# Optimization experiments

Hardware: AMD Instinct MI355X
Metric: run time of the kernel (lower is better)

The kernel has to match this reference:

```python
import jax, jax.numpy as jnp
import numpy as np

LMAX = 2
NEG_SLOPE = 0.2
N, K = 8192, 32
C_IN, C_ATTN = 128, 128
HEADS, HDIM = 8, 32
RAD_CH = [128, 64, 64, 2 * C_ATTN * (LMAX + 1)]  # edge_channel_list + [768]

# e3nn real spherical harmonics, normalize=True, normalization='integral'
_C0 = 0.28209479177387814           # sqrt(1/(4*pi))
_C1 = 0.4886025119029199            # sqrt(3/(4*pi))
_C2 = 0.6307831305050401            # sqrt(5/(4*pi))
_S3 = 1.7320508075688772            # sqrt(3)

def _sh(l, u):
    x, y, z = u[..., 0], u[..., 1], u[..., 2]
    if l == 0:
        return jnp.full(u.shape[:-1] + (1,), _C0, dtype=u.dtype)
    if l == 1:
        return _C1 * jnp.stack([x, y, z], axis=-1)
    return _C2 * jnp.stack([
        _S3 * x * z,
        _S3 * x * y,
        y * y - 0.5 * (x * x + z * z),
        _S3 * y * z,
        0.5 * _S3 * (z * z - x * x),
    ], axis=-1)

def _layernorm(x, g, b, eps=1e-5):
    m = jnp.mean(x, axis=-1, keepdims=True)
    v = jnp.var(x, axis=-1, keepdims=True)
    return (x - m) * jax.lax.rsqrt(v + eps) * g + b

def _smooth_leaky_relu(x):
    # (1+a)/2 * x + (1-a)/2 * x * (2*sigmoid(x) - 1)
    return 0.5 * (1 + NEG_SLOPE) * x + 0.5 * (1 - NEG_SLOPE) * x * (2.0 * jax.nn.sigmoid(x) - 1.0)


def setup_inputs() -> dict:
    key = jax.random.key(0)
    ks = jax.random.split(key, 32)
    inp = {}
    inp['x_edge'] = jax.random.normal(ks[0], (N, K, RAD_CH[0]), jnp.float32)
    inp['node_irreps_input'] = jax.random.normal(ks[1], (N, (LMAX + 1) ** 2, C_IN), jnp.float32)
    inp['edge_vec'] = jax.random.normal(ks[2], (N, K, 3), jnp.float32)
    inp['f_sparse_idx_node'] = jax.random.randint(ks[3], (N, K), 0, N)
    # SO3_Linear: per-l weight [lmax+1, out, in], bias only for l=0
    inp['dot_w'] = jax.random.normal(ks[4], (LMAX + 1, C_ATTN, C_IN), jnp.float32) / np.sqrt(C_IN)
    inp['dot_b'] = jnp.zeros((C_ATTN,), jnp.float32)
    # RadialFunction: Linear-LN-SiLU, Linear-LN-SiLU, Linear
    for i in range(3):
        inp[f'rad_w{i}'] = jax.random.normal(ks[5 + i], (RAD_CH[i + 1], RAD_CH[i]), jnp.float32) / np.sqrt(RAD_CH[i])
        inp[f'rad_b{i}'] = jnp.zeros((RAD_CH[i + 1],), jnp.float32)
    for i in range(2):
        inp[f'rad_g{i}'] = jnp.ones((RAD_CH[i + 1],), jnp.float32)
        inp[f'rad_bb{i}'] = jnp.zeros((RAD_CH[i + 1],), jnp.float32)
    # fc_m0: 768 -> heads*head
    inp['fc_w'] = jax.random.normal(ks[10], (HEADS * HDIM, RAD_CH[-1]), jnp.float32) / np.sqrt(RAD_CH[-1])
    inp['fc_b'] = jnp.zeros((HEADS * HDIM,), jnp.float32)
    # alpha_norm (LayerNorm over attn_scalar_head)
    inp['ln_g'] = jnp.ones((HDIM,), jnp.float32)
    inp['ln_b'] = jnp.zeros((HDIM,), jnp.float32)
    # alpha_dot ~ U(-1/sqrt(head), 1/sqrt(head))
    std = 1.0 / np.sqrt(HDIM)
    inp['alpha_dot'] = jax.random.uniform(ks[11], (HEADS, HDIM), jnp.float32, -std, std)
    return inp


def reference(x_edge, node_irreps_input, edge_vec, f_sparse_idx_node,
              dot_w, dot_b, rad_w0, rad_b0, rad_w1, rad_b1, rad_w2, rad_b2,
              rad_g0, rad_bb0, rad_g1, rad_bb1, fc_w, fc_b, ln_g, ln_b, alpha_dot):
    n = node_irreps_input.shape[0]
    # normalize edge vectors (e3nn normalize=True)
    u = edge_vec / jnp.clip(jnp.linalg.norm(edge_vec, axis=-1, keepdims=True), 1e-12)
    feats = []
    for l in range(LMAX + 1):
        node_l = node_irreps_input[:, l * l:(l + 1) * (l + 1)]          # [N, 2l+1, C_in]
        node_l = jnp.einsum('nmc,dc->nmd', node_l, dot_w[l])            # [N, 2l+1, C_attn]
        if l == 0:
            node_l = node_l + dot_b
        sh = _sh(l, u)                                                   # [N, K, 2l+1]
        feats.append(jnp.einsum('nkm,nmd->nkd', sh, node_l))            # self term
        gathered = jnp.take(node_l, f_sparse_idx_node, axis=0)          # [N, K, 2l+1, C_attn]
        feats.append(jnp.einsum('nkm,nkmd->nkd', sh, gathered))         # neighbor term
    x0 = jnp.concatenate(feats, axis=-1)                                 # [N, K, 768]
    # radial MLP on edge scalars
    h = jax.nn.silu(_layernorm(x_edge @ rad_w0.T + rad_b0, rad_g0, rad_bb0))
    h = jax.nn.silu(_layernorm(h @ rad_w1.T + rad_b1, rad_g1, rad_bb1))
    edge_m0 = h @ rad_w2.T + rad_b2                                      # [N, K, 768]
    x0a = (x0 * edge_m0) @ fc_w.T + fc_b                                 # [N, K, H*Dh]
    x0a = x0a.reshape(n, -1, HEADS, HDIM)
    x0a = _smooth_leaky_relu(_layernorm(x0a, ln_g, ln_b))
    alpha = jnp.einsum('nkhd,hd->nkh', x0a, alpha_dot)                   # [N, K, H]
    return alpha
```

## Files before the change

### kernel.cpp

```cpp
#include <hip/hip_runtime.h>
#include <hip/hip_bf16.h>
#include <stdint.h>

typedef __hip_bfloat16 bf16_t;
typedef __attribute__((ext_vector_type(8))) short bfrag8;
typedef __attribute__((ext_vector_type(4))) float facc4;

__device__ __forceinline__ float bfu(unsigned short s) {
  union { unsigned int i; float f; } u; u.i = ((unsigned int)s) << 16; return u.f;
}
__device__ __forceinline__ float2 bfup(unsigned int v) {
  union { unsigned int i; float f; } a, b;
  a.i = v << 16;
  b.i = v & 0xffff0000u;
  float2 r; r.x = a.f; r.y = b.f; return r;
}
__device__ __forceinline__ unsigned short f2b(float f) {
  __hip_bfloat16 h = __float2bfloat16(f);
  return *(unsigned short*)&h;
}
__device__ __forceinline__ void gload_lds16(const void* g, void* l) {
  __builtin_amdgcn_global_load_lds(
      (const __attribute__((address_space(1))) unsigned int*)g,
      (__attribute__((address_space(3))) unsigned int*)l, 16, 0, 0);
}

template<bool BF>
__device__ __forceinline__ float ld1(const void* p, size_t i) {
  if (BF) return bfu(((const unsigned short*)p)[i]);
  return ((const float*)p)[i];
}
template<bool BF>
__device__ __forceinline__ void ld8(const void* p, size_t i, float* o) {
  if (BF) {
    uint4 v = *(const uint4*)((const unsigned short*)p + i);
    float2 a = bfup(v.x), b = bfup(v.y), c = bfup(v.z), d = bfup(v.w);
    o[0]=a.x; o[1]=a.y; o[2]=b.x; o[3]=b.y; o[4]=c.x; o[5]=c.y; o[6]=d.x; o[7]=d.y;
  } else {
    float4 v0 = *(const float4*)((const float*)p + i);
    float4 v1 = *(const float4*)((const float*)p + i + 4);
    o[0]=v0.x; o[1]=v0.y; o[2]=v0.z; o[3]=v0.w; o[4]=v1.x; o[5]=v1.y; o[6]=v1.z; o[7]=v1.w;
  }
}
template<bool BF>
__device__ __forceinline__ void st1(void* p, size_t i, float v) {
  if (BF) ((unsigned short*)p)[i] = f2b(v);
  else    ((float*)p)[i] = v;
}
__device__ __forceinline__ bool tag_is_bf16(const void* ones) {
  return *(const unsigned int*)ones == 0x3F803F80u;
}

template<bool BF>
__global__ __launch_bounds__(256) void k_prep(
    const void* __restrict__ fcw, const void* __restrict__ w2,
    const void* __restrict__ lng,
    unsigned short* __restrict__ dstf, unsigned short* __restrict__ dstw2)
{
  if (tag_is_bf16(lng) != BF) return;
  int i = blockIdx.x * 256 + threadIdx.x;
  for (int e = i; e < 196608; e += 65536) dstf[e] = f2b(ld1<BF>(fcw, e));
  if (i < 49152) dstw2[i] = f2b(ld1<BF>(w2, i));
}

template<bool BF>
__global__ __launch_bounds__(128) void k_nodelin(
    const void* __restrict__ node, const void* __restrict__ dotw,
    const void* __restrict__ dotb, const void* __restrict__ lng,
    unsigned short* __restrict__ nlin)
{
  if (tag_is_bf16(lng) != BF) return;
  const int n = blockIdx.x, t = threadIdx.x;
  __shared__ alignas(16) float ns[1152];
  for (int i = t; i < 144; i += 128) ld8<BF>(node, (size_t)n * 1152 + i * 8, ns + i * 8);
  __syncthreads();
  unsigned short* outr = nlin + (size_t)n * 1152;
  #pragma unroll
  for (int l = 0; l < 3; ++l) {
    const int mb = l * l, mc = 2 * l + 1;
    float acc[5];
    #pragma unroll
    for (int mm = 0; mm < 5; ++mm) acc[mm] = 0.f;
    if (l == 0) acc[0] = ld1<BF>(dotb, t);
    #pragma unroll
    for (int c8 = 0; c8 < 16; ++c8) {
      float w[8]; ld8<BF>(dotw, (size_t)l * 16384 + (size_t)t * 128 + c8 * 8, w);
      #pragma unroll
      for (int mm = 0; mm < 5; ++mm) {
        if (mm < mc) {
          const float* sc = ns + (mb + mm) * 128 + c8 * 8;
          acc[mm] += sc[0]*w[0] + sc[1]*w[1] + sc[2]*w[2] + sc[3]*w[3]
                   + sc[4]*w[4] + sc[5]*w[5] + sc[6]*w[6] + sc[7]*w[7];
        }
      }
    }
    #pragma unroll
    for (int mm = 0; mm < 5; ++mm)
      if (mm < mc) outr[(mb + mm) * 128 + t] = f2b(acc[mm]);
  }
}

template<bool BF>
__global__ __launch_bounds__(256) void k_rad(
    const void* __restrict__ xe_g,
    const void* __restrict__ w0g, const void* __restrict__ b0g,
    const void* __restrict__ w1g, const void* __restrict__ b1g,
    const void* __restrict__ g0g, const void* __restrict__ bb0g,
    const void* __restrict__ g1g, const void* __restrict__ bb1g,
    const void* __restrict__ lng, unsigned short* __restrict__ h1g)
{
  if (tag_is_bf16(lng) != BF) return;
  const int t = threadIdx.x;
  const size_t ebase = (size_t)blockIdx.x * 64;
  __shared__ alignas(16) unsigned short xs [64 * 136];
  __shared__ alignas(16) unsigned short ws0[64 * 136];
  __shared__ alignas(16) unsigned short ws1[64 * 72];
  __shared__ alignas(16) unsigned short hs [64 * 72];

  for (int i8 = t; i8 < 1024; i8 += 256) {
    float v[8]; ld8<BF>(xe_g, (ebase + (i8 >> 4)) * 128 + (i8 & 15) * 8, v);
    unsigned short* d = &xs[(i8 >> 4) * 136 + (i8 & 15) * 8];
    #pragma unroll
    for (int j = 0; j < 8; ++j) d[j] = f2b(v[j]);
  }
  for (int i8 = t; i8 < 1024; i8 += 256) {
    float v[8]; ld8<BF>(w0g, (size_t)(i8 >> 4) * 128 + (i8 & 15) * 8, v);
    unsigned short* d = &ws0[(i8 >> 4) * 136 + (i8 & 15) * 8];
    #pragma unroll
    for (int j = 0; j < 8; ++j) d[j] = f2b(v[j]);
  }
  for (int i8 = t; i8 < 512; i8 += 256) {
    float v[8]; ld8<BF>(w1g, (size_t)(i8 >> 3) * 64 + (i8 & 7) * 8, v);
    unsigned short* d = &ws1[(i8 >> 3) * 72 + (i8 & 7) * 8];
    #pragma unroll
    for (int j = 0; j < 8; ++j) d[j] = f2b(v[j]);
  }
  __syncthreads();

  const int wv = t >> 6, lane = t & 63, la = lane & 15, qa = lane >> 4;
  facc4 acc[4];
  #pragma unroll
  for (int nt = 0; nt < 4; ++nt) acc[nt] = (facc4){0.f, 0.f, 0.f, 0.f};
  #pragma unroll
  for (int ks = 0; ks < 4; ++ks) {
    const int kk = ks * 32 + qa * 8;
    bfrag8 a = *(const bfrag8*)&xs[(wv * 16 + la) * 136 + kk];
    #pragma unroll
    for (int nt = 0; nt < 4; ++nt) {
      bfrag8 b = *(const bfrag8*)&ws0[(nt * 16 + la) * 136 + kk];
      acc[nt] = __builtin_amdgcn_mfma_f32_16x16x32_bf16(a, b, acc[nt], 0, 0, 0);
    }
  }
  {
    float bz[4], g[4], bb[4];
    #pragma unroll
    for (int nt = 0; nt < 4; ++nt) {
      const int ch = nt * 16 + la;
      bz[nt] = ld1<BF>(b0g, ch); g[nt] = ld1<BF>(g0g, ch); bb[nt] = ld1<BF>(bb0g, ch);
    }
    #pragma unroll
    for (int r = 0; r < 4; ++r) {
      float v[4], s = 0.f, s2 = 0.f;
      #pragma unroll
      for (int nt = 0; nt < 4; ++nt) { v[nt] = acc[nt][r] + bz[nt]; s += v[nt]; s2 += v[nt]*v[nt]; }
      #pragma unroll
      for (int msk = 1; msk < 16; msk <<= 1) { s += __shfl_xor(s, msk, 64); s2 += __shfl_xor(s2, msk, 64); }
      float mean = s * (1.f / 64.f);
      float var  = fmaxf(s2 * (1.f / 64.f) - mean * mean, 0.f);
      float rs   = rsqrtf(var + 1e-5f);
      const int er = wv * 16 + qa * 4 + r;
      #pragma unroll
      for (int nt = 0; nt < 4; ++nt) {
        float x = (v[nt] - mean) * rs * g[nt] + bb[nt];
        hs[er * 72 + nt * 16 + la] = f2b(x / (1.f + __expf(-x)));
      }
    }
  }
  __syncthreads();
  facc4 acc2[4];
  #pragma unroll
  for (int nt = 0; nt < 4; ++nt) acc2[nt] = (facc4){0.f, 0.f, 0.f, 0.f};
  #pragma unroll
  for (int ks = 0; ks < 2; ++ks) {
    const int kk = ks * 32 + qa * 8;
    bfrag8 a = *(const bfrag8*)&hs[(wv * 16 + la) * 72 + kk];
    #pragma unroll
    for (int nt = 0; nt < 4; ++nt) {
      bfrag8 b = *(const bfrag8*)&ws1[(nt * 16 + la) * 72 + kk];
      acc2[nt] = __builtin_amdgcn_mfma_f32_16x16x32_bf16(a, b, acc2[nt], 0, 0, 0);
    }
  }
  {
    float bz[4], g[4], bb[4];
    #pragma unroll
    for (int nt = 0; nt < 4; ++nt) {
      const int ch = nt * 16 + la;
      bz[nt] = ld1<BF>(b1g, ch); g[nt] = ld1<BF>(g1g, ch); bb[nt] = ld1<BF>(bb1g, ch);
    }
    #pragma unroll
    for (int r = 0; r < 4; ++r) {
      float v[4], s = 0.f, s2 = 0.f;
      #pragma unroll
      for (int nt = 0; nt < 4; ++nt) { v[nt] = acc2[nt][r] + bz[nt]; s += v[nt]; s2 += v[nt]*v[nt]; }
      #pragma unroll
      for (int msk = 1; msk < 16; msk <<= 1) { s += __shfl_xor(s, msk, 64); s2 += __shfl_xor(s2, msk, 64); }
      float mean = s * (1.f / 64.f);
      float var  = fmaxf(s2 * (1.f / 64.f) - mean * mean, 0.f);
      float rs   = rsqrtf(var + 1e-5f);
      const size_t er = ebase + wv * 16 + qa * 4 + r;
      #pragma unroll
      for (int nt = 0; nt < 4; ++nt) {
        float x = (v[nt] - mean) * rs * g[nt] + bb[nt];
        h1g[er * 64 + nt * 16 + la] = f2b(x / (1.f + __expf(-x)));
      }
    }
  }
}

template<bool BF>
__global__ __launch_bounds__(256, 4) void k_y(
    const void* __restrict__ evec, const int* __restrict__ idxg,
    const unsigned short* __restrict__ nlin, const unsigned short* __restrict__ h1g,
    const unsigned short* __restrict__ w2bf, const void* __restrict__ b2g,
    const void* __restrict__ lng,
    int node0, unsigned short* __restrict__ yg)
{
  if (tag_is_bf16(lng) != BF) return;
  const int nloc = blockIdx.x;
  const int n = node0 + nloc;
  const int t = threadIdx.x;
  __shared__ alignas(16) unsigned short h1_s[32 * 72];
  __shared__ alignas(16) float sh_s[32][9];
  __shared__ alignas(16) int idx_s[32];
  __shared__ alignas(16) float x0g[3][16 * 132];

  if (t < 32) {
    idx_s[t] = idxg[n * 32 + t];
    size_t eo = (size_t)(n * 32 + t) * 3;
    float x = ld1<BF>(evec, eo), y = ld1<BF>(evec, eo + 1), z = ld1<BF>(evec, eo + 2);
    float r = fmaxf(sqrtf(x * x + y * y + z * z), 1e-12f);
    float inv = 1.f / r; x *= inv; y *= inv; z *= inv;
    const float C1 = 0.4886025119029199f, C2 = 0.6307831305050401f, S3 = 1.7320508075688772f;
    sh_s[t][0] = 0.28209479177387814f;
    sh_s[t][1] = C1 * x; sh_s[t][2] = C1 * y; sh_s[t][3] = C1 * z;
    sh_s[t][4] = C2 * S3 * x * z;
    sh_s[t][5] = C2 * S3 * x * y;
    sh_s[t][6] = C2 * (y * y - 0.5f * (x * x + z * z));
    sh_s[t][7] = C2 * S3 * y * z;
    sh_s[t][8] = C2 * 0.5f * S3 * (z * z - x * x);
  }
  {
    int e = t >> 3, c = (t & 7) * 8;
    *(uint4*)&h1_s[e * 72 + c] = *(const uint4*)(h1g + ((size_t)n * 32 + e) * 64 + c);
  }
  __syncthreads();

  const int wv = t >> 6, lane = t & 63, la = lane & 15, qa = lane >> 4;
  const int dbase0 = wv * 192;
  unsigned short* yb = yg + (size_t)nloc * 32 * 768;

  #pragma unroll 1
  for (int half = 0; half < 2; ++half) {
    #pragma unroll 1
    for (int pass = 0; pass < 4; ++pass) {
      const int kl = pass * 4 + (t >> 6);
      const int ke = half * 16 + kl;
      const int dd0 = (t & 63) * 2;
      const unsigned short* rp = nlin + (size_t)idx_s[ke] * 1152 + dd0;
      const float* sh = sh_s[ke];
      unsigned int v; float2 f;
      v = *(const unsigned int*)(rp + 0 * 128); f = bfup(v);
      float s0x = sh[0] * f.x, s0y = sh[0] * f.y;
      v = *(const unsigned int*)(rp + 1 * 128); f = bfup(v);
      float s1x = sh[1] * f.x, s1y = sh[1] * f.y;
      v = *(const unsigned int*)(rp + 2 * 128); f = bfup(v);
      s1x += sh[2] * f.x; s1y += sh[2] * f.y;
      v = *(const unsigned int*)(rp + 3 * 128); f = bfup(v);
      s1x += sh[3] * f.x; s1y += sh[3] * f.y;
      v = *(const unsigned int*)(rp + 4 * 128); f = bfup(v);
      float s2x = sh[4] * f.x, s2y = sh[4] * f.y;
      v = *(const unsigned int*)(rp + 5 * 128); f = bfup(v);
      s2x += sh[5] * f.x; s2y += sh[5] * f.y;
      v = *(const unsigned int*)(rp + 6 * 128); f = bfup(v);
      s2x += sh[6] * f.x; s2y += sh[6] * f.y;
      v = *(const unsigned int*)(rp + 7 * 128); f = bfup(v);
      s2x += sh[7] * f.x; s2y += sh[7] * f.y;
      v = *(const unsigned int*)(rp + 8 * 128); f = bfup(v);
      s2x += sh[8] * f.x; s2y += sh[8] * f.y;
      float* p0 = &x0g[0][kl * 132 + dd0];
      float* p1 = &x0g[1][kl * 132 + dd0];
      float* p2 = &x0g[2][kl * 132 + dd0];
      p0[0] = s0x; p0[1] = s0y;
      p1[0] = s1x; p1[1] = s1y;
      p2[0] = s2x; p2[1] = s2y;
    }
    __syncthreads();

    const bfrag8 ah0 = *(const bfrag8*)&h1_s[(half * 16 + la) * 72 + qa * 8];
    const bfrag8 ah1 = *(const bfrag8*)&h1_s[(half * 16 + la) * 72 + 32 + qa * 8];
    #pragma unroll 1
    for (int nt = 0; nt < 12; ++nt) {
      const int d = dbase0 + nt * 16 + la;
      const int b = (dbase0 + nt * 16) >> 7;
      const int l = b >> 1;
      const bool gat = b & 1;
      const int mbase = l * l;
      const int mcnt = 2 * l + 1;
      const int dd = d & 127;

      facc4 acc = (facc4){0.f, 0.f, 0.f, 0.f};
      {
        bfrag8 bfr0 = *(const bfrag8*)(w2bf + (size_t)d * 64 + qa * 8);
        bfrag8 bfr1 = *(const bfrag8*)(w2bf + (size_t)d * 64 + 32 + qa * 8);
        acc = __builtin_amdgcn_mfma_f32_16x16x32_bf16(ah0, bfr0, acc, 0, 0, 0);
        acc = __builtin_amdgcn_mfma_f32_16x16x32_bf16(ah1, bfr1, acc, 0, 0, 0);
      }
      const float bias = ld1<BF>(b2g, d);

      if (!gat) {
        float pv[5];
        #pragma unroll
        for (int mm = 0; mm < 5; ++mm)
          pv[mm] = (mm < mcnt) ? bfu(nlin[(size_t)n * 1152 + (mbase + mm) * 128 + dd]) : 0.f;
        #pragma unroll
        for (int r = 0; r < 4; ++r) {
          const int kl = qa * 4 + r;
          const int ke = half * 16 + kl;
          float x0 = 0.f;
          #pragma unroll
          for (int mm = 0; mm < 5; ++mm)
            x0 += ((mm < mcnt) ? sh_s[ke][mbase + mm] : 0.f) * pv[mm];
          yb[(size_t)ke * 768 + d] = f2b(x0 * (acc[r] + bias));
        }
      } else {
        const float* xl = x0g[l];
        #pragma unroll
        for (int r = 0; r < 4; ++r) {
          const int kl = qa * 4 + r;
          const float x0 = xl[kl * 132 + dd];
          yb[(size_t)(half * 16 + kl) * 768 + d] = f2b(x0 * (acc[r] + bias));
        }
      }
    }
    __syncthreads();
  }
}

template<bool BF>
__global__ __launch_bounds__(256, 4) void k_fc2(
    const unsigned short* __restrict__ yg, const unsigned short* __restrict__ fcwbf,
    const void* __restrict__ fcb, const void* __restrict__ lng,
    const void* __restrict__ lnb, const void* __restrict__ adot,
    int node0, void* __restrict__ out)
{
  if (tag_is_bf16(lng) != BF) return;
  const int t = threadIdx.x;
  const int nb = blockIdx.y;
  __shared__ alignas(16) unsigned short a_s[128 * 64];
  __shared__ alignas(16) unsigned short b_s[128 * 64];

  const int wv = t >> 6, wm = wv >> 1, wn = wv & 1;
  const int lane = t & 63, la = lane & 15, qa = lane >> 4;
  const int lrow = lane >> 3, lg = lane & 7;

  facc4 acc[4][4];
  #pragma unroll
  for (int mt = 0; mt < 4; ++mt)
    #pragma unroll
    for (int nt = 0; nt < 4; ++nt) acc[mt][nt] = (facc4){0.f, 0.f, 0.f, 0.f};

  const unsigned short* abase = yg + (size_t)blockIdx.x * 128 * 768;
  const unsigned short* bbase = fcwbf + (size_t)nb * 128 * 768;

  #pragma unroll 1
  for (int kb = 0; kb < 12; ++kb) {
    #pragma unroll
    for (int j = 0; j < 4; ++j) {
      const int rbase = (wv * 4 + j) * 8;
      const int row = rbase + lrow;
      const int gs = (lg ^ (row & 7)) * 8;
      gload_lds16(abase + (size_t)row * 768 + kb * 64 + gs, &a_s[rbase * 64]);
    }
    #pragma unroll
    for (int j = 0; j < 4; ++j) {
      const int rbase = (wv * 4 + j) * 8;
      const int row = rbase + lrow;
      const int gs = (lg ^ (row & 7)) * 8;
      gload_lds16(bbase + (size_t)row * 768 + kb * 64 + gs, &b_s[rbase * 64]);
    }
    __syncthreads();
    #pragma unroll
    for (int ks = 0; ks < 2; ++ks) {
      const int g = ks * 4 + qa;
      bfrag8 af[4];
      #pragma unroll
      for (int mt = 0; mt < 4; ++mt) {
        const int ar = wm * 64 + mt * 16 + la;
        af[mt] = *(const bfrag8*)&a_s[ar * 64 + (g ^ (ar & 7)) * 8];
      }
      #pragma unroll
      for (int nt = 0; nt < 4; ++nt) {
        const int br = wn * 64 + nt * 16 + la;
        bfrag8 bf = *(const bfrag8*)&b_s[br * 64 + (g ^ (br & 7)) * 8];
        #pragma unroll
        for (int mt = 0; mt < 4; ++mt)
          acc[mt][nt] = __builtin_amdgcn_mfma_f32_16x16x32_bf16(af[mt], bf, acc[mt][nt], 0, 0, 0);
      }
    }
    __syncthreads();
  }

  const float gl0 = ld1<BF>(lng, la), gl1 = ld1<BF>(lng, la + 16);
  const float bl0 = ld1<BF>(lnb, la), bl1 = ld1<BF>(lnb, la + 16);
  const size_t e0 = (size_t)node0 * 32 + (size_t)blockIdx.x * 128 + wm * 64;
  #pragma unroll
  for (int hh = 0; hh < 2; ++hh) {
    const int hgl = nb * 4 + wn * 2 + hh;
    const float fb0 = ld1<BF>(fcb, hgl * 32 + la);
    const float fb1 = ld1<BF>(fcb, hgl * 32 + 16 + la);
    const float ad0 = ld1<BF>(adot, hgl * 32 + la);
    const float ad1 = ld1<BF>(adot, hgl * 32 + 16 + la);
    #pragma unroll
    for (int mt = 0; mt < 4; ++mt) {
      #pragma unroll
      for (int r = 0; r < 4; ++r) {
        float v0 = acc[mt][2 * hh][r] + fb0;
        float v1 = acc[mt][2 * hh + 1][r] + fb1;
        float s = v0 + v1, s2 = v0 * v0 + v1 * v1;
        #pragma unroll
        for (int msk = 1; msk < 16; msk <<= 1) {
          s  += __shfl_xor(s,  msk, 64);
          s2 += __shfl_xor(s2, msk, 64);
        }
        float mean = s * (1.f / 32.f);
        float var  = fmaxf(s2 * (1.f / 32.f) - mean * mean, 0.f);
        float rs   = rsqrtf(var + 1e-5f);
        float x0n = (v0 - mean) * rs * gl0 + bl0;
        float x1n = (v1 - mean) * rs * gl1 + bl1;
        float sg0 = 1.f / (1.f + __expf(-x0n));
        float sg1 = 1.f / (1.f + __expf(-x1n));
        float p = (0.6f * x0n + 0.4f * x0n * (2.f * sg0 - 1.f)) * ad0
                + (0.6f * x1n + 0.4f * x1n * (2.f * sg1 - 1.f)) * ad1;
        #pragma unroll
        for (int msk = 1; msk < 16; msk <<= 1) p += __shfl_xor(p, msk, 64);
        if (la == 0) {
          const size_t e = e0 + mt * 16 + qa * 4 + r;
          st1<BF>(out, e * 8 + hgl, p);
        }
      }
    }
  }
}

template<bool BF>
__global__ __launch_bounds__(256) void k_edge2(
    const void* __restrict__ evec, const int* __restrict__ idxg,
    const unsigned short* __restrict__ nlin, const unsigned short* __restrict__ fcwbf,
    const unsigned short* __restrict__ h1g,
    const void* __restrict__ w2g, const void* __restrict__ b2g,
    const void* __restrict__ fcb, const void* __restrict__ lng,
    const void* __restrict__ lnb, const void* __restrict__ adot,
    void* __restrict__ out)
{
  if (tag_is_bf16(lng) != BF) return;
  const int n = blockIdx.x, t = threadIdx.x;
  __shared__ alignas(16) unsigned short y_s[32 * 776];
  __shared__ alignas(16) unsigned short h1_s[32 * 72];
  __shared__ alignas(16) float sh_s[32][9];
  __shared__ alignas(16) int idx_s[32];

  if (t < 32) {
    idx_s[t] = idxg[n * 32 + t];
    size_t eo = (size_t)(n * 32 + t) * 3;
    float x = ld1<BF>(evec, eo), y = ld1<BF>(evec, eo + 1), z = ld1<BF>(evec, eo + 2);
    float r = fmaxf(sqrtf(x * x + y * y + z * z), 1e-12f);
    float inv = 1.f / r; x *= inv; y *= inv; z *= inv;
    const float C1 = 0.4886025119029199f, C2 = 0.6307831305050401f, S3 = 1.7320508075688772f;
    sh_s[t][0] = 0.28209479177387814f;
    sh_s[t][1] = C1 * x; sh_s[t][2] = C1 * y; sh_s[t][3] = C1 * z;
    sh_s[t][4] = C2 * S3 * x * z;
    sh_s[t][5] = C2 * S3 * x * y;
    sh_s[t][6] = C2 * (y * y - 0.5f * (x * x + z * z));
    sh_s[t][7] = C2 * S3 * y * z;
    sh_s[t][8] = C2 * 0.5f * S3 * (z * z - x * x);
  }
  if (t < 256) {
    int i8 = t;
    int e = i8 >> 3, c = (i8 & 7) * 8;
    uint4 v = *(const uint4*)(h1g + ((size_t)n * 32 + e) * 64 + c);
    *(uint4*)&h1_s[e * 72 + c] = v;
  }
  __syncthreads();

  for (int rep = 0; rep < 3; ++rep) {
    const int d = t + rep * 256;
    const int b = d >> 7, dd = d & 127;
    const int l = b >> 1;
    const bool gat = b & 1;
    const int mbase = l * l;
    const int mcnt = 2 * l + 1;
    const float bias = ld1<BF>(b2g, d);
    for (int kh = 0; kh < 2; ++kh) {
      float em[16];
      #pragma unroll
      for (int k = 0; k < 16; ++k) em[k] = bias;
      #pragma unroll
      for (int c8 = 0; c8 < 8; ++c8) {
        float w[8]; ld8<BF>(w2g, (size_t)d * 64 + c8 * 8, w);
        #pragma unroll
        for (int k = 0; k < 16; ++k) {
          uint4 hv = *(const uint4*)&h1_s[(kh * 16 + k) * 72 + c8 * 8];
          float2 a0 = bfup(hv.x), a1 = bfup(hv.y), a2 = bfup(hv.z), a3 = bfup(hv.w);
          em[k] += a0.x*w[0] + a0.y*w[1] + a1.x*w[2] + a1.y*w[3]
                 + a2.x*w[4] + a2.y*w[5] + a3.x*w[6] + a3.y*w[7];
        }
      }
      if (!gat) {
        const unsigned short* p = nlin + (size_t)n * 1152 + mbase * 128 + dd;
        float pv[5];
        #pragma unroll
        for (int mm = 0; mm < 5; ++mm) pv[mm] = (mm < mcnt) ? bfu(p[mm * 128]) : 0.f;
        #pragma unroll
        for (int k = 0; k < 16; ++k) {
          const int ke = kh * 16 + k;
          float x0 = 0.f;
          #pragma unroll
          for (int mm = 0; mm < 5; ++mm)
            x0 += ((mm < mcnt) ? sh_s[ke][mbase + mm] : 0.f) * pv[mm];
          y_s[ke * 776 + d] = f2b(x0 * em[k]);
        }
      } else {
        #pragma unroll 4
        for (int k = 0; k < 16; ++k) {
          const int ke = kh * 16 + k;
          const unsigned short* p = nlin + (size_t)idx_s[ke] * 1152 + mbase * 128 + dd;
          float x0 = 0.f;
          #pragma unroll
          for (int mm = 0; mm < 5; ++mm)
            x0 += ((mm < mcnt) ? sh_s[ke][mbase + mm] : 0.f) * bfu(p[mm * 128]);
          y_s[ke * 776 + d] = f2b(x0 * em[k]);
        }
      }
    }
  }
  __syncthreads();

  {
    const int wv = t >> 6, lane = t & 63;
    const int la = lane & 15, qa = lane >> 4;
    facc4 acc[2][4];
    #pragma unroll
    for (int mt = 0; mt < 2; ++mt)
      #pragma unroll
      for (int nt = 0; nt < 4; ++nt) acc[mt][nt] = (facc4){0.f, 0.f, 0.f, 0.f};
    for (int ks = 0; ks < 24; ++ks) {
      const int kk = ks * 32 + qa * 8;
      bfrag8 a0 = *(const bfrag8*)&y_s[la * 776 + kk];
      bfrag8 a1 = *(const bfrag8*)&y_s[(la + 16) * 776 + kk];
      #pragma unroll
      for (int nt = 0; nt < 4; ++nt) {
        bfrag8 bf = *(const bfrag8*)(fcwbf + (size_t)(wv * 64 + nt * 16 + la) * 768 + kk);
        acc[0][nt] = __builtin_amdgcn_mfma_f32_16x16x32_bf16(a0, bf, acc[0][nt], 0, 0, 0);
        acc[1][nt] = __builtin_amdgcn_mfma_f32_16x16x32_bf16(a1, bf, acc[1][nt], 0, 0, 0);
      }
    }
    const float gl0 = ld1<BF>(lng, la), gl1 = ld1<BF>(lng, la + 16);
    const float bl0 = ld1<BF>(lnb, la), bl1 = ld1<BF>(lnb, la + 16);
    #pragma unroll
    for (int hh = 0; hh < 2; ++hh) {
      const int hgl = wv * 2 + hh;
      const float fb0 = ld1<BF>(fcb, wv * 64 + hh * 32 + la);
      const float fb1 = ld1<BF>(fcb, wv * 64 + hh * 32 + 16 + la);
      const float ad0 = ld1<BF>(adot, hgl * 32 + la);
      const float ad1 = ld1<BF>(adot, hgl * 32 + 16 + la);
      #pragma unroll
      for (int mt = 0; mt < 2; ++mt) {
        #pragma unroll
        for (int r = 0; r < 4; ++r) {
          float v0 = acc[mt][2 * hh][r] + fb0;
          float v1 = acc[mt][2 * hh + 1][r] + fb1;
          float s = v0 + v1, s2 = v0 * v0 + v1 * v1;
          #pragma unroll
          for (int msk = 1; msk < 16; msk <<= 1) {
            s  += __shfl_xor(s,  msk, 64);
            s2 += __shfl_xor(s2, msk, 64);
          }
          float mean = s * (1.f / 32.f);
          float var  = fmaxf(s2 * (1.f / 32.f) - mean * mean, 0.f);
          float rs   = rsqrtf(var + 1e-5f);
          float x0n = (v0 - mean) * rs * gl0 + bl0;
          float x1n = (v1 - mean) * rs * gl1 + bl1;
          float sg0 = 1.f / (1.f + __expf(-x0n));
          float sg1 = 1.f / (1.f + __expf(-x1n));
          float p = (0.6f * x0n + 0.4f * x0n * (2.f * sg0 - 1.f)) * ad0
                  + (0.6f * x1n + 0.4f * x1n * (2.f * sg1 - 1.f)) * ad1;
          #pragma unroll
          for (int msk = 1; msk < 16; msk <<= 1) p += __shfl_xor(p, msk, 64);
          if (la == 0) {
            const int k = mt * 16 + qa * 4 + r;
            st1<BF>(out, (size_t)n * 256 + k * 8 + hgl, p);
          }
        }
      }
    }
  }
}

template<bool BF>
__global__ __launch_bounds__(256) void k_edge_fb(
    const void* __restrict__ xe_g, const void* __restrict__ evec,
    const int* __restrict__ idxg,
    const void* __restrict__ nodeg, const void* __restrict__ dotw,
    const void* __restrict__ dotb,
    const void* __restrict__ w0g, const void* __restrict__ b0g,
    const void* __restrict__ w1g, const void* __restrict__ b1g,
    const void* __restrict__ w2g, const void* __restrict__ b2g,
    const void* __restrict__ g0g, const void* __restrict__ bb0g,
    const void* __restrict__ g1g, const void* __restrict__ bb1g,
    const void* __restrict__ fcw, const void* __restrict__ fcb,
    const void* __restrict__ lng, const void* __restrict__ lnb,
    const void* __restrict__ adot, void* __restrict__ out)
{
  if (tag_is_bf16(lng) != BF) return;
  const int n = blockIdx.x, t = threadIdx.x;
  __shared__ alignas(16) char yb[32 * 776 * 2];
  __shared__ alignas(16) float sh_s[32][9];
  __shared__ alignas(16) int idx_s[32];
  __shared__ alignas(16) float mu_s[32], rs_s[32];
  __shared__ alignas(16) unsigned short h0_s[32][72];
  __shared__ alignas(16) unsigned short h1_s[32][72];
  unsigned short* y_s  = (unsigned short*)yb;
  unsigned short* xe_s = (unsigned short*)yb;
  float* zbuf = (float*)(yb + 8960);

  if (t < 32) {
    idx_s[t] = idxg[n * 32 + t];
    size_t eo = (size_t)(n * 32 + t) * 3;
    float x = ld1<BF>(evec, eo), y = ld1<BF>(evec, eo + 1), z = ld1<BF>(evec, eo + 2);
    float r = fmaxf(sqrtf(x * x + y * y + z * z), 1e-12f);
    float inv = 1.f / r; x *= inv; y *= inv; z *= inv;
    const float C1 = 0.4886025119029199f, C2 = 0.6307831305050401f, S3 = 1.7320508075688772f;
    sh_s[t][0] = 0.28209479177387814f;
    sh_s[t][1] = C1 * x; sh_s[t][2] = C1 * y; sh_s[t][3] = C1 * z;
    sh_s[t][4] = C2 * S3 * x * z;
    sh_s[t][5] = C2 * S3 * x * y;
    sh_s[t][6] = C2 * (y * y - 0.5f * (x * x + z * z));
    sh_s[t][7] = C2 * S3 * y * z;
    sh_s[t][8] = C2 * 0.5f * S3 * (z * z - x * x);
  }
  for (int i8 = t; i8 < 512; i8 += 256) {
    float v[8]; ld8<BF>(xe_g, (size_t)n * 4096 + i8 * 8, v);
    int k = i8 >> 4, c = (i8 & 15) * 8;
    unsigned short* dst = &xe_s[k * 136 + c];
    #pragma unroll
    for (int j = 0; j < 8; ++j) dst[j] = f2b(v[j]);
  }
  __syncthreads();
  const int k1 = t >> 3, j0 = (t & 7) * 8;
  float zr[8];
  #pragma unroll
  for (int jj = 0; jj < 8; ++jj) {
    const int j = j0 + jj;
    float acc = ld1<BF>(b0g, j);
    #pragma unroll
    for (int c8 = 0; c8 < 16; ++c8) {
      float w[8]; ld8<BF>(w0g, (size_t)j * 128 + c8 * 8, w);
      uint4 xv = *(const uint4*)&xe_s[k1 * 136 + c8 * 8];
      float2 a0 = bfup(xv.x), a1 = bfup(xv.y), a2 = bfup(xv.z), a3 = bfup(xv.w);
      acc += a0.x*w[0] + a0.y*w[1] + a1.x*w[2] + a1.y*w[3]
           + a2.x*w[4] + a2.y*w[5] + a3.x*w[6] + a3.y*w[7];
    }
    zr[jj] = acc;
  }
  __syncthreads();
  #pragma unroll
  for (int jj = 0; jj < 8; ++jj) zbuf[k1 * 64 + j0 + jj] = zr[jj];
  __syncthreads();
  if (t < 32) {
    const float* z = zbuf + t * 64;
    float s = 0.f, s2 = 0.f;
    for (int c = 0; c < 64; ++c) { float v = z[c]; s += v; s2 += v * v; }
    float m = s * (1.f / 64.f);
    float var = fmaxf(s2 * (1.f / 64.f) - m * m, 0.f);
    mu_s[t] = m; rs_s[t] = rsqrtf(var + 1e-5f);
  }
  __syncthreads();
  {
    float m = mu_s[k1], rs = rs_s[k1];
    #pragma unroll
    for (int jj = 0; jj < 8; ++jj) {
      int j = j0 + jj;
      float v = (zr[jj] - m) * rs * ld1<BF>(g0g, j) + ld1<BF>(bb0g, j);
      h0_s[k1][j] = f2b(v / (1.f + __expf(-v)));
    }
  }
  __syncthreads();
  #pragma unroll
  for (int jj = 0; jj < 8; ++jj) {
    const int j = j0 + jj;
    float acc = ld1<BF>(b1g, j);
    #pragma unroll
    for (int c8 = 0; c8 < 8; ++c8) {
      float w[8]; ld8<BF>(w1g, (size_t)j * 64 + c8 * 8, w);
      uint4 hv = *(const uint4*)&h0_s[k1][c8 * 8];
      float2 a0 = bfup(hv.x), a1 = bfup(hv.y), a2 = bfup(hv.z), a3 = bfup(hv.w);
      acc += a0.x*w[0] + a0.y*w[1] + a1.x*w[2] + a1.y*w[3]
           + a2.x*w[4] + a2.y*w[5] + a3.x*w[6] + a3.y*w[7];
    }
    zr[jj] = acc;
    zbuf[k1 * 64 + j] = acc;
  }
  __syncthreads();
  if (t < 32) {
    const float* z = zbuf + t * 64;
    float s = 0.f, s2 = 0.f;
    for (int c = 0; c < 64; ++c) { float v = z[c]; s += v; s2 += v * v; }
    float m = s * (1.f / 64.f);
    float var = fmaxf(s2 * (1.f / 64.f) - m * m, 0.f);
    mu_s[t] = m; rs_s[t] = rsqrtf(var + 1e-5f);
  }
  __syncthreads();
  {
    float m = mu_s[k1], rs = rs_s[k1];
    #pragma unroll
    for (int jj = 0; jj < 8; ++jj) {
      int j = j0 + jj;
      float v = (zr[jj] - m) * rs * ld1<BF>(g1g, j) + ld1<BF>(bb1g, j);
      h1_s[k1][j] = f2b(v / (1.f + __expf(-v)));
    }
  }
  __syncthreads();
  for (int rep = 0; rep < 3; ++rep) {
    const int d = t + rep * 256;
    const int b = d >> 7, dd = d & 127;
    const int l = b >> 1;
    const bool gat = b & 1;
    const int mbase = l * l;
    const int mcnt = 2 * l + 1;
    const float bias = ld1<BF>(b2g, d);
    for (int kh = 0; kh < 2; ++kh) {
      float em[16];
      #pragma unroll
      for (int k = 0; k < 16; ++k) em[k] = bias;
      #pragma unroll
      for (int c8 = 0; c8 < 8; ++c8) {
        float w[8]; ld8<BF>(w2g, (size_t)d * 64 + c8 * 8, w);
        #pragma unroll
        for (int k = 0; k < 16; ++k) {
          uint4 hv = *(const uint4*)&h1_s[kh * 16 + k][c8 * 8];
          float2 a0 = bfup(hv.x), a1 = bfup(hv.y), a2 = bfup(hv.z), a3 = bfup(hv.w);
          em[k] += a0.x*w[0] + a0.y*w[1] + a1.x*w[2] + a1.y*w[3]
                 + a2.x*w[4] + a2.y*w[5] + a3.x*w[6] + a3.y*w[7];
        }
      }
      const float db = (l == 0) ? ld1<BF>(dotb, dd) : 0.f;
      const size_t wbase = ((size_t)l * 128 + dd) * 128;
      if (!gat) {
        float pv[5];
        #pragma unroll
        for (int mm = 0; mm < 5; ++mm) {
          float a = 0.f;
          if (mm < mcnt) {
            #pragma unroll
            for (int c8 = 0; c8 < 16; ++c8) {
              float w[8]; ld8<BF>(dotw, wbase + c8 * 8, w);
              float x[8]; ld8<BF>(nodeg, (size_t)n * 1152 + (size_t)(mbase + mm) * 128 + c8 * 8, x);
              a += x[0]*w[0] + x[1]*w[1] + x[2]*w[2] + x[3]*w[3]
                 + x[4]*w[4] + x[5]*w[5] + x[6]*w[6] + x[7]*w[7];
            }
            if (mbase + mm == 0) a += db;
          }
          pv[mm] = a;
        }
        #pragma unroll
        for (int k = 0; k < 16; ++k) {
          const int ke = kh * 16 + k;
          float x0 = 0.f;
          #pragma unroll
          for (int mm = 0; mm < 5; ++mm)
            x0 += ((mm < mcnt) ? sh_s[ke][mbase + mm] : 0.f) * pv[mm];
          y_s[ke * 776 + d] = f2b(x0 * em[k]);
        }
      } else {
        for (int k = 0; k < 16; ++k) {
          const int ke = kh * 16 + k;
          float x0 = 0.f;
          for (int mm = 0; mm < mcnt; ++mm) {
            float a = 0.f;
            #pragma unroll
            for (int c8 = 0; c8 < 16; ++c8) {
              float w[8]; ld8<BF>(dotw, wbase + c8 * 8, w);
              float x[8]; ld8<BF>(nodeg, (size_t)idx_s[ke] * 1152 + (size_t)(mbase + mm) * 128 + c8 * 8, x);
              a += x[0]*w[0] + x[1]*w[1] + x[2]*w[2] + x[3]*w[3]
                 + x[4]*w[4] + x[5]*w[5] + x[6]*w[6] + x[7]*w[7];
            }
            if (mbase + mm == 0) a += db;
            x0 += sh_s[ke][mbase + mm] * a;
          }
          y_s[ke * 776 + d] = f2b(x0 * em[k]);
        }
      }
    }
  }
  __syncthreads();
  {
    const int wv = t >> 6, lane = t & 63;
    const int la = lane & 15, qa = lane >> 4;
    facc4 acc[2][4];
    #pragma unroll
    for (int mt = 0; mt < 2; ++mt)
      #pragma unroll
      for (int nt = 0; nt < 4; ++nt) acc[mt][nt] = (facc4){0.f, 0.f, 0.f, 0.f};
    for (int ks = 0; ks < 24; ++ks) {
      const int kk = ks * 32 + qa * 8;
      bfrag8 a0 = *(const bfrag8*)&y_s[la * 776 + kk];
      bfrag8 a1 = *(const bfrag8*)&y_s[(la + 16) * 776 + kk];
      #pragma unroll
      for (int nt = 0; nt < 4; ++nt) {
        bfrag8 bf;
        float v[8]; ld8<BF>(fcw, (size_t)(wv * 64 + nt * 16 + la) * 768 + kk, v);
        #pragma unroll
        for (int j = 0; j < 8; ++j) ((unsigned short*)&bf)[j] = f2b(v[j]);
        acc[0][nt] = __builtin_amdgcn_mfma_f32_16x16x32_bf16(a0, bf, acc[0][nt], 0, 0, 0);
        acc[1][nt] = __builtin_amdgcn_mfma_f32_16x16x32_bf16(a1, bf, acc[1][nt], 0, 0, 0);
      }
    }
    const float gl0 = ld1<BF>(lng, la), gl1 = ld1<BF>(lng, la + 16);
    const float bl0 = ld1<BF>(lnb, la), bl1 = ld1<BF>(lnb, la + 16);
    #pragma unroll
    for (int hh = 0; hh < 2; ++hh) {
      const int hgl = wv * 2 + hh;
      const float fb0 = ld1<BF>(fcb, wv * 64 + hh * 32 + la);
      const float fb1 = ld1<BF>(fcb, wv * 64 + hh * 32 + 16 + la);
      const float ad0 = ld1<BF>(adot, hgl * 32 + la);
      const float ad1 = ld1<BF>(adot, hgl * 32 + 16 + la);
      #pragma unroll
      for (int mt = 0; mt < 2; ++mt) {
        #pragma unroll
        for (int r = 0; r < 4; ++r) {
          float v0 = acc[mt][2 * hh][r] + fb0;
          float v1 = acc[mt][2 * hh + 1][r] + fb1;
          float s = v0 + v1, s2 = v0 * v0 + v1 * v1;
          #pragma unroll
          for (int msk = 1; msk < 16; msk <<= 1) {
            s  += __shfl_xor(s,  msk, 64);
            s2 += __shfl_xor(s2, msk, 64);
          }
          float mean = s * (1.f / 32.f);
          float var  = fmaxf(s2 * (1.f / 32.f) - mean * mean, 0.f);
          float rs   = rsqrtf(var + 1e-5f);
          float x0n = (v0 - mean) * rs * gl0 + bl0;
          float x1n = (v1 - mean) * rs * gl1 + bl1;
          float sg0 = 1.f / (1.f + __expf(-x0n));
          float sg1 = 1.f / (1.f + __expf(-x1n));
          float p = (0.6f * x0n + 0.4f * x0n * (2.f * sg0 - 1.f)) * ad0
                  + (0.6f * x1n + 0.4f * x1n * (2.f * sg1 - 1.f)) * ad1;
          #pragma unroll
          for (int msk = 1; msk < 16; msk <<= 1) p += __shfl_xor(p, msk, 64);
          if (la == 0) {
            const int k = mt * 16 + qa * 4 + r;
            st1<BF>(out, (size_t)n * 256 + k * 8 + hgl, p);
          }
        }
      }
    }
  }
}

extern "C" void kernel_launch(void* const* d_in, const int* in_sizes, int n_in,
                              void* d_out, int out_size, void* d_ws, size_t ws_size,
                              hipStream_t stream) {
  const void* x_edge = d_in[0];
  const void* node   = d_in[1];
  const void* evec   = d_in[2];
  const int*  idx    = (const int*)d_in[3];
  const void* dotw = d_in[4];
  const void* dotb = d_in[5];
  const void* w0  = d_in[6];
  const void* b0  = d_in[7];
  const void* w1  = d_in[8];
  const void* b1  = d_in[9];
  const void* w2  = d_in[10];
  const void* b2  = d_in[11];
  const void* g0  = d_in[12];
  const void* bb0 = d_in[13];
  const void* g1  = d_in[14];
  const void* bb1 = d_in[15];
  const void* fcw = d_in[16];
  const void* fcb = d_in[17];
  const void* lng = d_in[18];
  const void* lnb = d_in[19];
  const void* adot = d_in[20];

  const size_t NLIN = (size_t)8192 * 1152;
  const size_t FCW  = 196608;
  const size_t W2E  = 49152;
  const size_t H1   = (size_t)262144 * 64;
  const size_t need = (NLIN + FCW + W2E + H1) * sizeof(unsigned short);
  unsigned short* nlin  = (unsigned short*)d_ws;
  unsigned short* fcwbf = nlin + NLIN;
  unsigned short* w2bf  = fcwbf + FCW;
  unsigned short* h1g   = w2bf + W2E;
  unsigned short* yg    = h1g + H1;

  if (ws_size >= need) {
    k_nodelin<true ><<<dim3(8192), dim3(128), 0, stream>>>(node, dotw, dotb, lng, nlin);
    k_nodelin<false><<<dim3(8192), dim3(128), 0, stream>>>(node, dotw, dotb, lng, nlin);
    k_prep<true ><<<dim3(256), dim3(256), 0, stream>>>(fcw, w2, lng, fcwbf, w2bf);
    k_prep<false><<<dim3(256), dim3(256), 0, stream>>>(fcw, w2, lng, fcwbf, w2bf);
    k_rad<true ><<<dim3(4096), dim3(256), 0, stream>>>(x_edge, w0, b0, w1, b1, g0, bb0, g1, bb1, lng, h1g);
    k_rad<false><<<dim3(4096), dim3(256), 0, stream>>>(x_edge, w0, b0, w1, b1, g0, bb0, g1, bb1, lng, h1g);

    size_t avail = ws_size - need;
    long chunk = (long)(avail / ((size_t)32 * 768 * 2));
    if (chunk > 8192) chunk = 8192;
    chunk &= ~3L;
    if (chunk >= 512) {
      for (long n0 = 0; n0 < 8192; n0 += chunk) {
        int g = (int)(((8192 - n0) < chunk) ? (8192 - n0) : chunk);
        k_y<true ><<<dim3(g), dim3(256), 0, stream>>>(evec, idx, nlin, h1g, w2bf, b2, lng, (int)n0, yg);
        k_y<false><<<dim3(g), dim3(256), 0, stream>>>(evec, idx, nlin, h1g, w2bf, b2, lng, (int)n0, yg);
        k_fc2<true ><<<dim3(g / 4, 2), dim3(256), 0, stream>>>(yg, fcwbf, fcb, lng, lnb, adot, (int)n0, d_out);
        k_fc2<false><<<dim3(g / 4, 2), dim3(256), 0, stream>>>(yg, fcwbf, fcb, lng, lnb, adot, (int)n0, d_out);
      }
    } else {
      k_edge2<true ><<<dim3(8192), dim3(256), 0, stream>>>(
          evec, idx, nlin, fcwbf, h1g, w2, b2, fcb, lng, lnb, adot, d_out);
      k_edge2<false><<<dim3(8192), dim3(256), 0, stream>>>(
          evec, idx, nlin, fcwbf, h1g, w2, b2, fcb, lng, lnb, adot, d_out);
    }
  } else {
    k_edge_fb<true ><<<dim3(8192), dim3(256), 0, stream>>>(
        x_edge, evec, idx, node, dotw, dotb, w0, b0, w1, b1, w2, b2,
        g0, bb0, g1, bb1, fcw, fcb, lng, lnb, adot, d_out);
    k_edge_fb<false><<<dim3(8192), dim3(256), 0, stream>>>(
        x_edge, evec, idx, node, dotw, dotb, w0, b0, w1, b1, w2, b2,
        g0, bb0, g1, bb1, fcw, fcb, lng, lnb, adot, d_out);
  }
}
```

Before: 1.009 ms.

## Batch 4 nodes per nodelin block and transpose k_y MFMA for vectorized stores

k_nodelin now processes four nodes per block, so each weight row read from global memory is reused across four nodes, with a quarter as many blocks. k_y swaps the MFMA operands so each lane holds four consecutive output channels for one edge, which allows packed 8-byte stores, float4 reads of the gathered features and 4-wide loads of nlin and the bias. The next tile's W2 fragments and bias are prefetched a step ahead. Occupancy hints are raised to 5 waves and the pass loop is partially unrolled, at the cost of more register pressure.

Result: faster. 922.1 us (-8.6%).

```diff
diff --git a/kernel.cpp b/kernel.cpp
--- a/kernel.cpp
+++ b/kernel.cpp
@@ -29,6 +29,17 @@
 __device__ __forceinline__ float ld1(const void* p, size_t i) {
   if (BF) return bfu(((const unsigned short*)p)[i]);
   return ((const float*)p)[i];
+}
+template<bool BF>
+__device__ __forceinline__ void ld4(const void* p, size_t i, float* o) {
+  if (BF) {
+    uint2 v = *(const uint2*)((const unsigned short*)p + i);
+    float2 a = bfup(v.x), b = bfup(v.y);
+    o[0]=a.x; o[1]=a.y; o[2]=b.x; o[3]=b.y;
+  } else {
+    float4 v = *(const float4*)((const float*)p + i);
+    o[0]=v.x; o[1]=v.y; o[2]=v.z; o[3]=v.w;
+  }
 }
 template<bool BF>
 __device__ __forceinline__ void ld8(const void* p, size_t i, float* o) {
@@ -70,33 +81,41 @@
     unsigned short* __restrict__ nlin)
 {
   if (tag_is_bf16(lng) != BF) return;
-  const int n = blockIdx.x, t = threadIdx.x;
-  __shared__ alignas(16) float ns[1152];
-  for (int i = t; i < 144; i += 128) ld8<BF>(node, (size_t)n * 1152 + i * 8, ns + i * 8);
-  __syncthreads();
-  unsigned short* outr = nlin + (size_t)n * 1152;
-  #pragma unroll
+  const int n0 = blockIdx.x * 4, t = threadIdx.x;
+  __shared__ alignas(16) float ns[4 * 1152];
+  for (int i = t; i < 576; i += 128) ld8<BF>(node, (size_t)n0 * 1152 + i * 8, ns + i * 8);
+  __syncthreads();
+  const float bias = ld1<BF>(dotb, t);
+  #pragma unroll 1
   for (int l = 0; l < 3; ++l) {
     const int mb = l * l, mc = 2 * l + 1;
-    float acc[5];
-    #pragma unroll
-    for (int mm = 0; mm < 5; ++mm) acc[mm] = 0.f;
-    if (l == 0) acc[0] = ld1<BF>(dotb, t);
-    #pragma unroll
+    float acc[4][5];
+    #pragma unroll
+    for (int j = 0; j < 4; ++j) {
+      #pragma unroll
+      for (int mm = 0; mm < 5; ++mm) acc[j][mm] = 0.f;
+      if (l == 0) acc[j][0] = bias;
+    }
+    #pragma unroll 2
     for (int c8 = 0; c8 < 16; ++c8) {
       float w[8]; ld8<BF>(dotw, (size_t)l * 16384 + (size_t)t * 128 + c8 * 8, w);
       #pragma unroll
-      for (int mm = 0; mm < 5; ++mm) {
-        if (mm < mc) {
-          const float* sc = ns + (mb + mm) * 128 + c8 * 8;
-          acc[mm] += sc[0]*w[0] + sc[1]*w[1] + sc[2]*w[2] + sc[3]*w[3]
-                   + sc[4]*w[4] + sc[5]*w[5] + sc[6]*w[6] + sc[7]*w[7];
-        }
-      }
-    }
-    #pragma unroll
-    for (int mm = 0; mm < 5; ++mm)
-      if (mm < mc) outr[(mb + mm) * 128 + t] = f2b(acc[mm]);
+      for (int j = 0; j < 4; ++j) {
+        #pragma unroll
+        for (int mm = 0; mm < 5; ++mm) {
+          if (mm < mc) {
+            const float* sc = ns + j * 1152 + (mb + mm) * 128 + c8 * 8;
+            acc[j][mm] += sc[0]*w[0] + sc[1]*w[1] + sc[2]*w[2] + sc[3]*w[3]
+                        + sc[4]*w[4] + sc[5]*w[5] + sc[6]*w[6] + sc[7]*w[7];
+          }
+        }
+      }
+    }
+    #pragma unroll
+    for (int j = 0; j < 4; ++j)
+      #pragma unroll
+      for (int mm = 0; mm < 5; ++mm)
+        if (mm < mc) nlin[(size_t)(n0 + j) * 1152 + (mb + mm) * 128 + t] = f2b(acc[j][mm]);
   }
 }
 
@@ -218,7 +237,7 @@
 }
 
 template<bool BF>
-__global__ __launch_bounds__(256, 4) void k_y(
+__global__ __launch_bounds__(256, 5) void k_y(
     const void* __restrict__ evec, const int* __restrict__ idxg,
     const unsigned short* __restrict__ nlin, const unsigned short* __restrict__ h1g,
     const unsigned short* __restrict__ w2bf, const void* __restrict__ b2g,
@@ -261,7 +280,7 @@
 
   #pragma unroll 1
   for (int half = 0; half < 2; ++half) {
-    #pragma unroll 1
+    #pragma unroll 2
     for (int pass = 0; pass < 4; ++pass) {
       const int kl = pass * 4 + (t >> 6);
       const int ke = half * 16 + kl;
@@ -296,51 +315,66 @@
     }
     __syncthreads();
 
-    const bfrag8 ah0 = *(const bfrag8*)&h1_s[(half * 16 + la) * 72 + qa * 8];
-    const bfrag8 ah1 = *(const bfrag8*)&h1_s[(half * 16 + la) * 72 + 32 + qa * 8];
+    const int ke = half * 16 + la;
+    const float* shk = sh_s[ke];
+    unsigned short* yrow = yb + (size_t)ke * 768;
+    const bfrag8 bh0 = *(const bfrag8*)&h1_s[ke * 72 + qa * 8];
+    const bfrag8 bh1 = *(const bfrag8*)&h1_s[ke * 72 + 32 + qa * 8];
+    bfrag8 na0 = *(const bfrag8*)(w2bf + (size_t)(dbase0 + la) * 64 + qa * 8);
+    bfrag8 na1 = *(const bfrag8*)(w2bf + (size_t)(dbase0 + la) * 64 + 32 + qa * 8);
+    float nbias[4]; ld4<BF>(b2g, dbase0 + qa * 4, nbias);
     #pragma unroll 1
     for (int nt = 0; nt < 12; ++nt) {
-      const int d = dbase0 + nt * 16 + la;
-      const int b = (dbase0 + nt * 16) >> 7;
+      const int dtile = dbase0 + nt * 16;
+      const int b = dtile >> 7;
       const int l = b >> 1;
       const bool gat = b & 1;
       const int mbase = l * l;
       const int mcnt = 2 * l + 1;
-      const int dd = d & 127;
-
-      facc4 acc = (facc4){0.f, 0.f, 0.f, 0.f};
-      {
-        bfrag8 bfr0 = *(const bfrag8*)(w2bf + (size_t)d * 64 + qa * 8);
-        bfrag8 bfr1 = *(const bfrag8*)(w2bf + (size_t)d * 64 + 32 + qa * 8);
-        acc = __builtin_amdgcn_mfma_f32_16x16x32_bf16(ah0, bfr0, acc, 0, 0, 0);
-        acc = __builtin_amdgcn_mfma_f32_16x16x32_bf16(ah1, bfr1, acc, 0, 0, 0);
-      }
-      const float bias = ld1<BF>(b2g, d);
-
+      const int d4 = dtile + qa * 4;
+      const int dd4 = d4 & 127;
+
+      const bfrag8 ca0 = na0, ca1 = na1;
+      float bias[4] = {nbias[0], nbias[1], nbias[2], nbias[3]};
+      if (nt < 11) {
+        na0 = *(const bfrag8*)(w2bf + (size_t)(dtile + 16 + la) * 64 + qa * 8);
+        na1 = *(const bfrag8*)(w2bf + (size_t)(dtile + 16 + la) * 64 + 32 + qa * 8);
+        ld4<BF>(b2g, dtile + 16 + qa * 4, nbias);
+      }
+
+      float x0[4];
       if (!gat) {
-        float pv[5];
-        #pragma unroll
-        for (int mm = 0; mm < 5; ++mm)
-          pv[mm] = (mm < mcnt) ? bfu(nlin[(size_t)n * 1152 + (mbase + mm) * 128 + dd]) : 0.f;
+        float pv[5][4];
+        #pragma unroll
+        for (int mm = 0; mm < 5; ++mm) {
+          if (mm < mcnt) ld4<true>(nlin, (size_t)n * 1152 + (mbase + mm) * 128 + dd4, pv[mm]);
+          else { pv[mm][0] = pv[mm][1] = pv[mm][2] = pv[mm][3] = 0.f; }
+        }
         #pragma unroll
         for (int r = 0; r < 4; ++r) {
-          const int kl = qa * 4 + r;
-          const int ke = half * 16 + kl;
-          float x0 = 0.f;
+          float s = 0.f;
           #pragma unroll
           for (int mm = 0; mm < 5; ++mm)
-            x0 += ((mm < mcnt) ? sh_s[ke][mbase + mm] : 0.f) * pv[mm];
-          yb[(size_t)ke * 768 + d] = f2b(x0 * (acc[r] + bias));
+            s += ((mm < mcnt) ? shk[mbase + mm] : 0.f) * pv[mm][r];
+          x0[r] = s;
         }
       } else {
-        const float* xl = x0g[l];
-        #pragma unroll
-        for (int r = 0; r < 4; ++r) {
-          const int kl = qa * 4 + r;
-          const float x0 = xl[kl * 132 + dd];
-          yb[(size_t)(half * 16 + kl) * 768 + d] = f2b(x0 * (acc[r] + bias));
-        }
-      }
+        float4 xv = *(const float4*)&x0g[l][la * 132 + dd4];
+        x0[0] = xv.x; x0[1] = xv.y; x0[2] = xv.z; x0[3] = xv.w;
+      }
+
+      facc4 acc = (facc4){0.f, 0.f, 0.f, 0.f};
+      acc = __builtin_amdgcn_mfma_f32_16x16x32_bf16(ca0, bh0, acc, 0, 0, 0);
+      acc = __builtin_amdgcn_mfma_f32_16x16x32_bf16(ca1, bh1, acc, 0, 0, 0);
+
+      unsigned short o0 = f2b(x0[0] * (acc[0] + bias[0]));
+      unsigned short o1 = f2b(x0[1] * (acc[1] + bias[1]));
+      unsigned short o2 = f2b(x0[2] * (acc[2] + bias[2]));
+      unsigned short o3 = f2b(x0[3] * (acc[3] + bias[3]));
+      uint2 ov;
+      ov.x = (unsigned int)o0 | ((unsigned int)o1 << 16);
+      ov.y = (unsigned int)o2 | ((unsigned int)o3 << 16);
+      *(uint2*)(yrow + d4) = ov;
     }
     __syncthreads();
   }
@@ -904,8 +938,8 @@
   unsigned short* yg    = h1g + H1;
 
   if (ws_size >= need) {
-    k_nodelin<true ><<<dim3(8192), dim3(128), 0, stream>>>(node, dotw, dotb, lng, nlin);
-    k_nodelin<false><<<dim3(8192), dim3(128), 0, stream>>>(node, dotw, dotb, lng, nlin);
+    k_nodelin<true ><<<dim3(2048), dim3(128), 0, stream>>>(node, dotw, dotb, lng, nlin);
+    k_nodelin<false><<<dim3(2048), dim3(128), 0, stream>>>(node, dotw, dotb, lng, nlin);
     k_prep<true ><<<dim3(256), dim3(256), 0, stream>>>(fcw, w2, lng, fcwbf, w2bf);
     k_prep<false><<<dim3(256), dim3(256), 0, stream>>>(fcw, w2, lng, fcwbf, w2bf);
     k_rad<true ><<<dim3(4096), dim3(256), 0, stream>>>(x_edge, w0, b0, w1, b1, g0, bb0, g1, bb1, lng, h1g);
```
